# Optimization experiments

Hardware: AMD Instinct MI355X
Metric: run time of the kernel (lower is better)

## Reference

```python
import jax, jax.numpy as jnp
import numpy as np

L, H, D, FF = 6, 16, 768, 3072
B, N = 4, 1023
HD = D // H  # 48
EPS = 1e-5


def _layernorm(x, w, b):
    m = jnp.mean(x, axis=-1, keepdims=True)
    v = jnp.mean((x - m) ** 2, axis=-1, keepdims=True)
    return (x - m) / jnp.sqrt(v + EPS) * w + b


def setup_inputs() -> dict:
    key = jax.random.key(0)
    ks = jax.random.split(key, 10)
    ratio = 2.0 ** (-8.0 / H)
    slopes = np.array([ratio ** (i + 1) for i in range(H)], dtype=np.float32)
    return {
        "cls_tokens": jax.random.normal(ks[0], (B, N, D), jnp.float32),
        "cls_token": jax.random.normal(ks[1], (1, 1, D), jnp.float32) * 0.02,
        "log_slopes": jnp.log(jnp.asarray(slopes)),
        "Wqkv": jax.random.normal(ks[2], (L, 3 * D, D), jnp.float32) * 0.02,
        "Wo": jax.random.normal(ks[3], (L, D, D), jnp.float32) * 0.02,
        "Wg": jax.random.normal(ks[4], (L, FF, D), jnp.float32) * 0.02,
        "Wu": jax.random.normal(ks[5], (L, FF, D), jnp.float32) * 0.02,
        "Wd": jax.random.normal(ks[6], (L, D, FF), jnp.float32) * 0.02,
        "ln1_w": jnp.ones((L, D), jnp.float32),
        "ln1_b": jnp.zeros((L, D), jnp.float32),
        "ln2_w": jnp.ones((L, D), jnp.float32),
        "ln2_b": jnp.zeros((L, D), jnp.float32),
        "fin_w": jnp.ones((D,), jnp.float32),
        "fin_b": jnp.zeros((D,), jnp.float32),
    }


def reference(cls_tokens, cls_token, log_slopes, Wqkv, Wo, Wg, Wu, Wd,
              ln1_w, ln1_b, ln2_w, ln2_b, fin_w, fin_b):
    b, n, dmodel = cls_tokens.shape
    S = n + 1
    # learnable ALiBi: -exp(log_slope) * |i - j|, shape (H, S, S)
    pos = jnp.arange(S)
    dist = jnp.abs(pos[None, :] - pos[:, None]).astype(cls_tokens.dtype)
    bias = -(jnp.exp(log_slopes)[:, None, None] * dist[None, :, :])

    x = jnp.concatenate([jnp.broadcast_to(cls_token, (b, 1, dmodel)), cls_tokens], axis=1)
    scale = 1.0 / jnp.sqrt(jnp.asarray(HD, x.dtype))

    for l in range(L):
        h = _layernorm(x, ln1_w[l], ln1_b[l])
        qkv = jnp.einsum('bsd,ed->bse', h, Wqkv[l]).reshape(b, S, 3, H, HD)
        qkv = qkv.transpose(2, 0, 3, 1, 4)  # (3, B, H, S, hd)
        q, k, v = qkv[0], qkv[1], qkv[2]
        scores = jnp.einsum('bhqd,bhkd->bhqk', q, k) * scale + bias[None]
        attn = jax.nn.softmax(scores, axis=-1)
        o = jnp.einsum('bhqk,bhkd->bhqd', attn, v)
        o = o.transpose(0, 2, 1, 3).reshape(b, S, dmodel)
        x = x + jnp.einsum('bsd,ed->bse', o, Wo[l])
        h = _layernorm(x, ln2_w[l], ln2_b[l])
        gate = jax.nn.silu(jnp.einsum('bsd,fd->bsf', h, Wg[l]))
        up = jnp.einsum('bsd,fd->bsf', h, Wu[l])
        x = x + jnp.einsum('bsf,df->bsd', gate * up, Wd[l])

    return _layernorm(x[:, 0, :], fin_w, fin_b)
```

## Files before the change

kernel.cpp:

```cpp
#include <hip/hip_runtime.h>
#include <hip/hip_bf16.h>

#define LNUM 6
#define HNUM 16
#define DMODEL 768
#define FFDIM 3072
#define BATCH 4
#define NTOK 1023
#define SEQ 1024
#define HD 48
#define EPS 1e-5f

typedef __hip_bfloat16 bf16;

__device__ __forceinline__ unsigned short f2bf_raw(float f) {
  bf16 h = __float2bfloat16(f);
  union { bf16 h; unsigned short s; } u; u.h = h; return u.s;
}

template <int CTRL>
__device__ __forceinline__ float dppf(float x) {
  return __int_as_float(__builtin_amdgcn_update_dpp(
      0, __float_as_int(x), CTRL, 0xf, 0xf, true));
}
__device__ __forceinline__ float row_max16(float x) {
  x = fmaxf(x, dppf<0xB1>(x));
  x = fmaxf(x, dppf<0x4E>(x));
  x = fmaxf(x, dppf<0x124>(x));
  x = fmaxf(x, dppf<0x128>(x));
  return x;
}
__device__ __forceinline__ float row_sum16(float x) {
  x += dppf<0xB1>(x);
  x += dppf<0x4E>(x);
  x += dppf<0x124>(x);
  x += dppf<0x128>(x);
  return x;
}

__device__ __forceinline__ void xcd_swz(int& bx, int& by) {
  const int gx = gridDim.x;
  const int lin = blockIdx.y * gx + blockIdx.x;
  const int cpx = (gx * gridDim.y) >> 3;
  const int w = (lin & 7) * cpx + (lin >> 3);
  bx = w % gx;
  by = w / gx;
}

__global__ __launch_bounds__(256) void concat_kernel(
    const float* __restrict__ cls_tokens, const float* __restrict__ cls_token,
    float* __restrict__ x) {
  size_t i = (size_t)blockIdx.x * blockDim.x + threadIdx.x;
  const size_t total = (size_t)BATCH * SEQ * DMODEL;
  if (i >= total) return;
  int d = (int)(i % DMODEL);
  size_t bs = i / DMODEL;
  int s = (int)(bs % SEQ);
  int b = (int)(bs / SEQ);
  float v;
  if (s == 0) v = cls_token[d];
  else v = cls_tokens[((size_t)b * NTOK + (s - 1)) * DMODEL + d];
  x[i] = v;
}

#define W_QKV4  442368
#define W_O4    147456
#define W_FF4   589824
__global__ __launch_bounds__(256) void convert_w_kernel(
    const float* __restrict__ wqkv, const float* __restrict__ wo,
    const float* __restrict__ wg, const float* __restrict__ wu,
    const float* __restrict__ wd, bf16* __restrict__ dst) {
  size_t i4 = (size_t)blockIdx.x * 256 + threadIdx.x;
  size_t off4 = i4;
  const float* src;
  if (off4 < W_QKV4) src = wqkv;
  else { off4 -= W_QKV4;
    if (off4 < W_O4) src = wo;
    else { off4 -= W_O4;
      if (off4 < W_FF4) src = wg;
      else { off4 -= W_FF4;
        if (off4 < W_FF4) src = wu;
        else { off4 -= W_FF4; src = wd; } } } }
  float4 v = ((const float4*)src)[off4];
  ushort4 o;
  o.x = f2bf_raw(v.x); o.y = f2bf_raw(v.y);
  o.z = f2bf_raw(v.z); o.w = f2bf_raw(v.w);
  ((ushort4*)dst)[i4] = o;
}

__device__ __forceinline__ void st_ln(float* p, float v) { *p = v; }
__device__ __forceinline__ void st_ln(bf16* p, float v) { *p = __float2bfloat16(v); }

template <typename OUT>
__global__ __launch_bounds__(256) void ln_kernel(
    const float* __restrict__ in, OUT* __restrict__ out,
    const float* __restrict__ w, const float* __restrict__ bias,
    size_t in_stride, size_t out_stride) {
  const int row = blockIdx.x;
  const int tid = threadIdx.x;
  const float* x = in + (size_t)row * in_stride;
  OUT* y = out + (size_t)row * out_stride;

  float v0 = x[tid], v1 = x[tid + 256], v2 = x[tid + 512];
  float s = v0 + v1 + v2;
  float sq = v0 * v0 + v1 * v1 + v2 * v2;

  __shared__ float s_sum[256];
  __shared__ float s_sq[256];
  s_sum[tid] = s;
  s_sq[tid] = sq;
  __syncthreads();
  for (int off = 128; off > 0; off >>= 1) {
    if (tid < off) {
      s_sum[tid] += s_sum[tid + off];
      s_sq[tid] += s_sq[tid + off];
    }
    __syncthreads();
  }
  const float inv_d = 1.0f / (float)DMODEL;
  float mean = s_sum[0] * inv_d;
  float var = s_sq[0] * inv_d - mean * mean;
  float rstd = rsqrtf(var + EPS);

  st_ln(y + tid,       (v0 - mean) * rstd * w[tid]       + bias[tid]);
  st_ln(y + tid + 256, (v1 - mean) * rstd * w[tid + 256] + bias[tid + 256]);
  st_ln(y + tid + 512, (v2 - mean) * rstd * w[tid + 512] + bias[tid + 512]);
}

#define BM 128
#define BN 128
#define BK 32

typedef __attribute__((ext_vector_type(8))) short bfrag;
typedef __attribute__((ext_vector_type(4))) float f32x4;

__device__ __forceinline__ void async_copy16(const void* g, void* l) {
  __builtin_amdgcn_global_load_lds(
      (const __attribute__((address_space(1))) void*)g,
      (__attribute__((address_space(3))) void*)l, 16, 0, 0);
}

template <int CMODE>
__global__ __launch_bounds__(256) void gemm_bf16(
    const bf16* __restrict__ A, const bf16* __restrict__ B,
    void* __restrict__ Cv, int M, int N, int K) {
  __shared__ bf16 As[2][BM][BK];
  __shared__ bf16 Bs[2][BN][BK];

  const int tid = threadIdx.x;
  const int wave = tid >> 6;
  const int lane = tid & 63;
  int bx, by;
  xcd_swz(bx, by);
  const int m0 = by * BM;
  const int n0 = bx * BN;
  const int wm = (wave & 1) * 64;
  const int wn = (wave >> 1) * 64;

  f32x4 acc[4][4];
#pragma unroll
  for (int i = 0; i < 4; i++)
#pragma unroll
    for (int j = 0; j < 4; j++) acc[i][j] = (f32x4)(0.f);

  const int lrow = lane >> 2;
  const int lcol = (lane & 3) * 8;
  const bf16* Ag[2]; const bf16* Bg[2];
  void *AsB[2][2], *BsB[2][2];
#pragma unroll
  for (int j = 0; j < 2; j++) {
    int c = j * 4 + wave;
    Ag[j] = A + (size_t)(m0 + c * 16 + lrow) * K + lcol;
    Bg[j] = B + (size_t)(n0 + c * 16 + lrow) * K + lcol;
#pragma unroll
    for (int bf = 0; bf < 2; bf++) {
      AsB[bf][j] = (void*)&As[bf][c * 16][0];
      BsB[bf][j] = (void*)&Bs[bf][c * 16][0];
    }
  }

#pragma unroll
  for (int j = 0; j < 2; j++) {
    async_copy16(Ag[j], AsB[0][j]);
    async_copy16(Bg[j], BsB[0][j]);
  }

  const int fr = lane & 15;
  const int fk = (lane >> 4) * 8;
  const int nk = K / BK;

  for (int ki = 0; ki < nk; ki++) {
    const int cur = ki & 1;
    __syncthreads();
    if (ki + 1 < nk) {
      const int k0 = (ki + 1) * BK;
#pragma unroll
      for (int j = 0; j < 2; j++) {
        async_copy16(Ag[j] + k0, AsB[cur ^ 1][j]);
        async_copy16(Bg[j] + k0, BsB[cur ^ 1][j]);
      }
    }
    bfrag a[4], b[4];
#pragma unroll
    for (int i = 0; i < 4; i++) {
      a[i] = *(const bfrag*)&As[cur][wm + i * 16 + fr][fk];
      b[i] = *(const bfrag*)&Bs[cur][wn + i * 16 + fr][fk];
    }
#pragma unroll
    for (int i = 0; i < 4; i++)
#pragma unroll
      for (int j = 0; j < 4; j++)
        acc[i][j] = __builtin_amdgcn_mfma_f32_16x16x32_bf16(a[i], b[j], acc[i][j], 0, 0, 0);
  }

  const int ccol = lane & 15;
  const int crow = (lane >> 4) * 4;
#pragma unroll
  for (int i = 0; i < 4; i++) {
#pragma unroll
    for (int j = 0; j < 4; j++) {
#pragma unroll
      for (int r = 0; r < 4; r++) {
        const size_t gm = m0 + wm + i * 16 + crow + r;
        const size_t gn = n0 + wn + j * 16 + ccol;
        if (CMODE == 2) {
          ((bf16*)Cv)[gm * N + gn] = __float2bfloat16(acc[i][j][r]);
        } else if (CMODE == 1) {
          float* cp = (float*)Cv + gm * N + gn;
          *cp += acc[i][j][r];
        } else {
          ((float*)Cv)[gm * N + gn] = acc[i][j][r];
        }
      }
    }
  }
}

template <int CMODE, int SPLITK>
__global__ __launch_bounds__(256) void gemm_bf16_n64(
    const bf16* __restrict__ A, const bf16* __restrict__ B,
    void* __restrict__ Cv, int M, int N, int K) {
  __shared__ bf16 As[2][64][BK];
  __shared__ bf16 Bs[2][64][BK];

  const int tid = threadIdx.x;
  const int wave = tid >> 6;
  const int lane = tid & 63;
  int bx, by;
  xcd_swz(bx, by);
  const int m0 = by * 64;
  const int n0 = bx * 64;
  const int wm = (wave & 1) * 32;
  const int wn = (wave >> 1) * 32;
  const int koff = (SPLITK > 1) ? (int)blockIdx.z * (K / SPLITK) : 0;

  f32x4 acc[2][2];
#pragma unroll
  for (int i = 0; i < 2; i++)
#pragma unroll
    for (int j = 0; j < 2; j++) acc[i][j] = (f32x4)(0.f);

  const int srow = tid >> 2;
  const int scol = (tid & 3) * 8;
  const bf16* Ag = A + (size_t)(m0 + srow) * K + koff + scol;
  const bf16* Bg = B + (size_t)(n0 + srow) * K + koff + scol;
  void *AsB[2], *BsB[2];
#pragma unroll
  for (int bf = 0; bf < 2; bf++) {
    AsB[bf] = (void*)&As[bf][srow][scol];
    BsB[bf] = (void*)&Bs[bf][srow][scol];
  }

  async_copy16(Ag, AsB[0]);
  async_copy16(Bg, BsB[0]);

  const int fr = lane & 15;
  const int fk = (lane >> 4) * 8;
  const int nk = (K / SPLITK) / BK;

  for (int ki = 0; ki < nk; ki++) {
    const int cur = ki & 1;
    __syncthreads();
    if (ki + 1 < nk) {
      const int k0 = (ki + 1) * BK;
      async_copy16(Ag + k0, AsB[cur ^ 1]);
      async_copy16(Bg + k0, BsB[cur ^ 1]);
    }
    bfrag a[2], b[2];
#pragma unroll
    for (int i = 0; i < 2; i++)
      a[i] = *(const bfrag*)&As[cur][wm + i * 16 + fr][fk];
#pragma unroll
    for (int j = 0; j < 2; j++)
      b[j] = *(const bfrag*)&Bs[cur][wn + j * 16 + fr][fk];
#pragma unroll
    for (int i = 0; i < 2; i++)
#pragma unroll
      for (int j = 0; j < 2; j++)
        acc[i][j] = __builtin_amdgcn_mfma_f32_16x16x32_bf16(a[i], b[j], acc[i][j], 0, 0, 0);
  }

  const int ccol = lane & 15;
  const int crow = (lane >> 4) * 4;
#pragma unroll
  for (int i = 0; i < 2; i++) {
#pragma unroll
    for (int j = 0; j < 2; j++) {
#pragma unroll
      for (int r = 0; r < 4; r++) {
        const size_t gm = m0 + wm + i * 16 + crow + r;
        const size_t gn = n0 + wn + j * 16 + ccol;
        if (CMODE == 2) {
          ((bf16*)Cv)[gm * N + gn] = __float2bfloat16(acc[i][j][r]);
        } else if (CMODE == 1) {
          float* cp = (float*)Cv + gm * N + gn;
          if (SPLITK > 1) atomicAdd(cp, acc[i][j][r]);
          else *cp += acc[i][j][r];
        } else {
          ((float*)Cv)[gm * N + gn] = acc[i][j][r];
        }
      }
    }
  }
}

__global__ __launch_bounds__(256) void gemm_gateup(
    const bf16* __restrict__ A, const bf16* __restrict__ Wg,
    const bf16* __restrict__ Wu, bf16* __restrict__ gu, int M, int N, int K) {
  __shared__ bf16 As[2][BM][BK];
  __shared__ bf16 Gs[2][BN][BK];
  __shared__ bf16 Us[2][BN][BK];

  const int tid = threadIdx.x;
  const int wave = tid >> 6;
  const int lane = tid & 63;
  int bx, by;
  xcd_swz(bx, by);
  const int m0 = by * BM;
  const int n0 = bx * BN;
  const int wm = (wave & 1) * 64;
  const int wn = (wave >> 1) * 64;

  f32x4 accG[4][4], accU[4][4];
#pragma unroll
  for (int i = 0; i < 4; i++)
#pragma unroll
    for (int j = 0; j < 4; j++) { accG[i][j] = (f32x4)(0.f); accU[i][j] = (f32x4)(0.f); }

  const int lrow = lane >> 2;
  const int lcol = (lane & 3) * 8;
  const bf16 *Ag[2], *Gg[2], *Ug[2];
  void *AsB[2][2], *GsB[2][2], *UsB[2][2];
#pragma unroll
  for (int j = 0; j < 2; j++) {
    int c = j * 4 + wave;
    Ag[j] = A + (size_t)(m0 + c * 16 + lrow) * K + lcol;
    Gg[j] = Wg + (size_t)(n0 + c * 16 + lrow) * K + lcol;
    Ug[j] = Wu + (size_t)(n0 + c * 16 + lrow) * K + lcol;
#pragma unroll
    for (int bf = 0; bf < 2; bf++) {
      AsB[bf][j] = (void*)&As[bf][c * 16][0];
      GsB[bf][j] = (void*)&Gs[bf][c * 16][0];
      UsB[bf][j] = (void*)&Us[bf][c * 16][0];
    }
  }

#pragma unroll
  for (int j = 0; j < 2; j++) {
    async_copy16(Ag[j], AsB[0][j]);
    async_copy16(Gg[j], GsB[0][j]);
    async_copy16(Ug[j], UsB[0][j]);
  }

  const int fr = lane & 15;
  const int fk = (lane >> 4) * 8;
  const int nk = K / BK;

  for (int ki = 0; ki < nk; ki++) {
    const int cur = ki & 1;
    __syncthreads();
    if (ki + 1 < nk) {
      const int k0 = (ki + 1) * BK;
#pragma unroll
      for (int j = 0; j < 2; j++) {
        async_copy16(Ag[j] + k0, AsB[cur ^ 1][j]);
        async_copy16(Gg[j] + k0, GsB[cur ^ 1][j]);
        async_copy16(Ug[j] + k0, UsB[cur ^ 1][j]);
      }
    }
    bfrag a[4], g[4], u[4];
#pragma unroll
    for (int i = 0; i < 4; i++) {
      a[i] = *(const bfrag*)&As[cur][wm + i * 16 + fr][fk];
      g[i] = *(const bfrag*)&Gs[cur][wn + i * 16 + fr][fk];
      u[i] = *(const bfrag*)&Us[cur][wn + i * 16 + fr][fk];
    }
#pragma unroll
    for (int i = 0; i < 4; i++)
#pragma unroll
      for (int j = 0; j < 4; j++) {
        accG[i][j] = __builtin_amdgcn_mfma_f32_16x16x32_bf16(a[i], g[j], accG[i][j], 0, 0, 0);
        accU[i][j] = __builtin_amdgcn_mfma_f32_16x16x32_bf16(a[i], u[j], accU[i][j], 0, 0, 0);
      }
  }

  const int ccol = lane & 15;
  const int crow = (lane >> 4) * 4;
#pragma unroll
  for (int i = 0; i < 4; i++) {
#pragma unroll
    for (int j = 0; j < 4; j++) {
#pragma unroll
      for (int r = 0; r < 4; r++) {
        const size_t gm = m0 + wm + i * 16 + crow + r;
        const size_t gn = n0 + wn + j * 16 + ccol;
        const float gv = accG[i][j][r];
        const float uv = accU[i][j][r];
        const float res = gv / (1.0f + __expf(-gv)) * uv;
        gu[gm * N + gn] = __float2bfloat16(res);
      }
    }
  }
}

__global__ __launch_bounds__(256) void transpose_v(
    const bf16* __restrict__ qkv, bf16* __restrict__ vt) {
  __shared__ bf16 T[HD][64];
  const int tid = threadIdx.x;
  const int kb = blockIdx.x * 64;
  const int h = blockIdx.y;
  const int b = blockIdx.z;
  const size_t rstride = 3 * DMODEL;
  const bf16* vsrc = qkv + ((size_t)(b * SEQ + kb)) * rstride + 2 * DMODEL + h * HD;

  if (tid < 192) {
    int p = tid & 31, c = tid >> 5;
    const bf16* v0 = vsrc + (size_t)(2 * p) * rstride + c * 8;
    uint4 r0 = *(const uint4*)v0;
    uint4 r1 = *(const uint4*)(v0 + rstride);
    const unsigned int* w0 = (const unsigned int*)&r0;
    const unsigned int* w1 = (const unsigned int*)&r1;
#pragma unroll
    for (int i = 0; i < 8; i++) {
      unsigned int lo = (i & 1) ? (w0[i >> 1] >> 16) : (w0[i >> 1] & 0xffffu);
      unsigned int hi = (i & 1) ? (w1[i >> 1] >> 16) : (w1[i >> 1] & 0xffffu);
      *(unsigned int*)&T[c * 8 + i][2 * p] = lo | (hi << 16);
    }
  }
  __syncthreads();
  for (int it = tid; it < HD * 8; it += 256) {
    int d = it >> 3, c = it & 7;
    *(uint4*)(vt + ((size_t)((b * HNUM + h) * HD + d)) * SEQ + kb + c * 8) =
        *(const uint4*)&T[d][c * 8];
  }
}

#define AQT 64
#define AKT 64
#define ASTR 72

__global__ __launch_bounds__(256, 4) void attn_mfma(
    const bf16* __restrict__ qkv, const bf16* __restrict__ vt,
    const float* __restrict__ log_slopes, bf16* __restrict__ obuf) {
  __shared__ bf16 QPs[AQT][ASTR];
  __shared__ bf16 Ks[AKT][ASTR];
  __shared__ bf16 Vs[HD][ASTR];

  const int tid = threadIdx.x;
  const int wq = tid >> 6;
  const int lane = tid & 63;
  const int l15 = lane & 15;
  const int lh = lane >> 4;

  const int id = blockIdx.x;
  const int w = (id & 7) * 128 + (id >> 3);
  const int qb = (w & 15) * AQT;
  const int h = (w >> 4) & 15;
  const int b = w >> 8;

  const float c1 = 0.14433756729740643f * 1.4426950408889634f;
  const float slope2 = __expf(log_slopes[h]) * 1.4426950408889634f;
  const size_t rstride = 3 * DMODEL;
  const bf16* qbase = qkv + ((size_t)(b * SEQ + qb)) * rstride + h * HD;
  const bf16* kbase0 = qkv + ((size_t)b * SEQ) * rstride + DMODEL + h * HD;
  const bf16* vbase0 = vt + ((size_t)((b * HNUM + h) * HD)) * SEQ;

  bf16* ldst[3];
  int goff[3];
  bool isK[3];
#pragma unroll
  for (int j = 0; j < 3; j++) {
    int id2 = tid + j * 256;
    if (id2 < 384) {
      int r = id2 / 6, c = id2 - r * 6;
      ldst[j] = &Ks[r][c * 8];
      goff[j] = r * (int)rstride + c * 8;
      isK[j] = true;
    } else {
      id2 -= 384;
      int d = id2 >> 3, c = id2 & 7;
      ldst[j] = &Vs[d][c * 8];
      goff[j] = d * SEQ + c * 8;
      isK[j] = false;
    }
  }

  for (int it = tid; it < AQT * 2; it += 256) {
    int r = it >> 1, c = it & 1;
    *(uint4*)&QPs[r][48 + c * 8] = make_uint4(0, 0, 0, 0);
    *(uint4*)&Ks[r][48 + c * 8] = make_uint4(0, 0, 0, 0);
  }
  for (int it = tid; it < AQT * 6; it += 256) {
    int r = it / 6, c = it - (it / 6) * 6;
    *(uint4*)&QPs[r][c * 8] = *(const uint4*)(qbase + (size_t)r * rstride + c * 8);
  }
  __syncthreads();
  const bfrag aq0 = *(const bfrag*)&QPs[wq * 16 + l15][lh * 8];
  const bfrag aq1 = *(const bfrag*)&QPs[wq * 16 + l15][32 + lh * 8];

  uint4 pre[3];
#pragma unroll
  for (int j = 0; j < 3; j++)
    pre[j] = *(const uint4*)((isK[j] ? kbase0 : vbase0) + goff[j]);

  float m_[4], l_[4];
  f32x4 accO[3];
#pragma unroll
  for (int r = 0; r < 4; r++) { m_[r] = -1e30f; l_[r] = 0.f; }
#pragma unroll
  for (int t = 0; t < 3; t++) accO[t] = (f32x4)(0.f);

  for (int kb = 0; kb < SEQ; kb += AKT) {
    __syncthreads();
#pragma unroll
    for (int j = 0; j < 3; j++) *(uint4*)ldst[j] = pre[j];
    __syncthreads();
    if (kb + AKT < SEQ) {
      const bf16* kb1 = kbase0 + (size_t)(kb + AKT) * rstride;
      const bf16* vb1 = vbase0 + (kb + AKT);
#pragma unroll
      for (int j = 0; j < 3; j++)
        pre[j] = *(const uint4*)((isK[j] ? kb1 : vb1) + goff[j]);
    }

    f32x4 accS[4];
#pragma unroll
    for (int j = 0; j < 4; j++) accS[j] = (f32x4)(0.f);
    __builtin_amdgcn_s_setprio(1);
#pragma unroll
    for (int j = 0; j < 4; j++) {
      bfrag bk = *(const bfrag*)&Ks[j * 16 + l15][lh * 8];
      accS[j] = __builtin_amdgcn_mfma_f32_16x16x32_bf16(aq0, bk, accS[j], 0, 0, 0);
    }
#pragma unroll
    for (int j = 0; j < 4; j++) {
      bfrag bk = *(const bfrag*)&Ks[j * 16 + l15][32 + lh * 8];
      accS[j] = __builtin_amdgcn_mfma_f32_16x16x32_bf16(aq1, bk, accS[j], 0, 0, 0);
    }
    __builtin_amdgcn_s_setprio(0);

    float ps[4][4];
#pragma unroll
    for (int r = 0; r < 4; r++) {
      const float fq = (float)(qb + wq * 16 + lh * 4 + r);
      float s[4];
#pragma unroll
      for (int j = 0; j < 4; j++) {
        const float fk = (float)(kb + j * 16 + l15);
        s[j] = fmaf(accS[j][r], c1, -slope2 * fabsf(fq - fk));
      }
      float mx = row_max16(fmaxf(fmaxf(s[0], s[1]), fmaxf(s[2], s[3])));
      if (!__all(mx - m_[r] <= 8.0f)) {
        const float mnew = fmaxf(m_[r], mx);
        const float corr = exp2f(m_[r] - mnew);
        l_[r] *= corr;
#pragma unroll
        for (int t = 0; t < 3; t++) accO[t][r] *= corr;
        m_[r] = mnew;
      }
      float rs = 0.f;
#pragma unroll
      for (int j = 0; j < 4; j++) {
        ps[j][r] = exp2f(s[j] - m_[r]);
        rs += ps[j][r];
      }
      rs = row_sum16(rs);
      l_[r] += rs;
    }

#pragma unroll
    for (int j = 0; j < 4; j++)
#pragma unroll
      for (int r = 0; r < 4; r++)
        QPs[wq * 16 + lh * 4 + r][j * 16 + l15] = __float2bfloat16(ps[j][r]);

#pragma unroll
    for (int ks = 0; ks < 2; ks++) {
      bfrag pa = *(const bfrag*)&QPs[wq * 16 + l15][ks * 32 + lh * 8];
      __builtin_amdgcn_s_setprio(1);
#pragma unroll
      for (int t = 0; t < 3; t++) {
        bfrag vb = *(const bfrag*)&Vs[t * 16 + l15][ks * 32 + lh * 8];
        accO[t] = __builtin_amdgcn_mfma_f32_16x16x32_bf16(pa, vb, accO[t], 0, 0, 0);
      }
      __builtin_amdgcn_s_setprio(0);
    }
  }

#pragma unroll
  for (int r = 0; r < 4; r++) {
    const float inv = 1.0f / l_[r];
    bf16* op = obuf + ((size_t)(b * SEQ + qb + wq * 16 + lh * 4 + r)) * DMODEL + h * HD;
#pragma unroll
    for (int t = 0; t < 3; t++)
      op[t * 16 + l15] = __float2bfloat16(accO[t][r] * inv);
  }
}

extern "C" void kernel_launch(void* const* d_in, const int* in_sizes, int n_in,
                              void* d_out, int out_size, void* d_ws, size_t ws_size,
                              hipStream_t stream) {
  const float* cls_tokens = (const float*)d_in[0];
  const float* cls_token  = (const float*)d_in[1];
  const float* log_slopes = (const float*)d_in[2];
  const float* Wqkv = (const float*)d_in[3];
  const float* Wo   = (const float*)d_in[4];
  const float* Wg   = (const float*)d_in[5];
  const float* Wu   = (const float*)d_in[6];
  const float* Wd   = (const float*)d_in[7];
  const float* ln1_w = (const float*)d_in[8];
  const float* ln1_b = (const float*)d_in[9];
  const float* ln2_w = (const float*)d_in[10];
  const float* ln2_b = (const float*)d_in[11];
  const float* fin_w = (const float*)d_in[12];
  const float* fin_b = (const float*)d_in[13];
  float* out = (float*)d_out;

  const size_t ROWS = (size_t)BATCH * SEQ;
  char* wsb = (char*)d_ws;
  float* x    = (float*)(wsb);
  bf16* qkvb  = (bf16*)(wsb + 12582912);
  bf16* hb    = (bf16*)(wsb + 31457280);
  bf16* ob    = (bf16*)(wsb + 37748736);
  bf16* gub   = (bf16*)(wsb + 44040192);
  bf16* wbf   = (bf16*)(wsb + 94371840);
  bf16* vtb   = (bf16*)(wsb + 113246208);

  bf16* wqkv_b = wbf;
  bf16* wo_b   = wbf + 1769472;
  bf16* wg_b   = wbf + 2359296;
  bf16* wu_b   = wbf + 4718592;
  bf16* wd_b   = wbf + 7077888;

  {
    const size_t total = ROWS * DMODEL;
    concat_kernel<<<(int)((total + 255) / 256), 256, 0, stream>>>(cls_tokens, cls_token, x);
  }

  for (int l = 0; l < LNUM; l++) {
    convert_w_kernel<<<9216, 256, 0, stream>>>(
        Wqkv + (size_t)l * 3 * DMODEL * DMODEL, Wo + (size_t)l * DMODEL * DMODEL,
        Wg + (size_t)l * FFDIM * DMODEL, Wu + (size_t)l * FFDIM * DMODEL,
        Wd + (size_t)l * DMODEL * FFDIM, wbf);

    ln_kernel<bf16><<<(int)ROWS, 256, 0, stream>>>(
        x, hb, ln1_w + l * DMODEL, ln1_b + l * DMODEL, DMODEL, DMODEL);
    gemm_bf16<2><<<dim3(3 * DMODEL / BN, ROWS / BM), 256, 0, stream>>>(
        hb, wqkv_b, qkvb, (int)ROWS, 3 * DMODEL, DMODEL);
    transpose_v<<<dim3(SEQ / 64, HNUM, BATCH), 256, 0, stream>>>(qkvb, vtb);
    attn_mfma<<<dim3(SEQ / AQT * HNUM * BATCH), 256, 0, stream>>>(
        qkvb, vtb, log_slopes, ob);
    gemm_bf16_n64<1, 1><<<dim3(DMODEL / 64, ROWS / 64), 256, 0, stream>>>(
        ob, wo_b, x, (int)ROWS, DMODEL, DMODEL);
    ln_kernel<bf16><<<(int)ROWS, 256, 0, stream>>>(
        x, hb, ln2_w + l * DMODEL, ln2_b + l * DMODEL, DMODEL, DMODEL);
    gemm_gateup<<<dim3(FFDIM / BN, ROWS / BM), 256, 0, stream>>>(
        hb, wg_b, wu_b, gub, (int)ROWS, FFDIM, DMODEL);
    gemm_bf16_n64<1, 2><<<dim3(DMODEL / 64, ROWS / 64, 2), 256, 0, stream>>>(
        gub, wd_b, x, (int)ROWS, DMODEL, FFDIM);
  }

  ln_kernel<float><<<BATCH, 256, 0, stream>>>(x, out, fin_w, fin_b,
                                              (size_t)SEQ * DMODEL, DMODEL);
}
```

Before: 1.765 ms.

## Split attention over KV halves, widen n64 GEMM tile, warp-per-row layernorm

Attention blocks now each process half of the key/value sequence and write unnormalized fp32 partial outputs plus running max/sum. A new combine kernel merges the two halves and writes bf16. This doubles the number of attention blocks for better occupancy, at the cost of extra fp32 traffic and one more launch. The n64 GEMM now uses 128-row tiles, and the Wo projection switches to split-K with atomic adds. Layernorm assigns one wave per row with float4 loads and shuffle reductions, replacing the shared-memory tree reduction.

```diff
diff --git a/kernel.cpp b/kernel.cpp
--- a/kernel.cpp
+++ b/kernel.cpp
@@ -88,43 +88,55 @@
   ((ushort4*)dst)[i4] = o;
 }
 
-__device__ __forceinline__ void st_ln(float* p, float v) { *p = v; }
-__device__ __forceinline__ void st_ln(bf16* p, float v) { *p = __float2bfloat16(v); }
+__device__ __forceinline__ void st4(float* p, float a, float b2, float c, float d) {
+  *(float4*)p = make_float4(a, b2, c, d);
+}
+__device__ __forceinline__ void st4(bf16* p, float a, float b2, float c, float d) {
+  ushort4 o;
+  o.x = f2bf_raw(a); o.y = f2bf_raw(b2); o.z = f2bf_raw(c); o.w = f2bf_raw(d);
+  *(ushort4*)p = o;
+}
 
 template <typename OUT>
 __global__ __launch_bounds__(256) void ln_kernel(
     const float* __restrict__ in, OUT* __restrict__ out,
     const float* __restrict__ w, const float* __restrict__ bias,
-    size_t in_stride, size_t out_stride) {
-  const int row = blockIdx.x;
-  const int tid = threadIdx.x;
+    size_t in_stride, size_t out_stride, int nrows) {
+  const int lane = threadIdx.x & 63;
+  const int row = blockIdx.x * 4 + (threadIdx.x >> 6);
+  if (row >= nrows) return;
   const float* x = in + (size_t)row * in_stride;
   OUT* y = out + (size_t)row * out_stride;
-
-  float v0 = x[tid], v1 = x[tid + 256], v2 = x[tid + 512];
-  float s = v0 + v1 + v2;
-  float sq = v0 * v0 + v1 * v1 + v2 * v2;
-
-  __shared__ float s_sum[256];
-  __shared__ float s_sq[256];
-  s_sum[tid] = s;
-  s_sq[tid] = sq;
-  __syncthreads();
-  for (int off = 128; off > 0; off >>= 1) {
-    if (tid < off) {
-      s_sum[tid] += s_sum[tid + off];
-      s_sq[tid] += s_sq[tid + off];
-    }
-    __syncthreads();
-  }
+  const int d = lane * 4;
+
+  float4 v0 = *(const float4*)(x + d);
+  float4 v1 = *(const float4*)(x + d + 256);
+  float4 v2 = *(const float4*)(x + d + 512);
+  float s = (v0.x + v0.y) + (v0.z + v0.w) + (v1.x + v1.y) + (v1.z + v1.w) +
+            (v2.x + v2.y) + (v2.z + v2.w);
+  float sq = v0.x * v0.x + v0.y * v0.y + v0.z * v0.z + v0.w * v0.w +
+             v1.x * v1.x + v1.y * v1.y + v1.z * v1.z + v1.w * v1.w +
+             v2.x * v2.x + v2.y * v2.y + v2.z * v2.z + v2.w * v2.w;
+  s = row_sum16(s);  s += __shfl_xor(s, 16, 64);  s += __shfl_xor(s, 32, 64);
+  sq = row_sum16(sq); sq += __shfl_xor(sq, 16, 64); sq += __shfl_xor(sq, 32, 64);
+
   const float inv_d = 1.0f / (float)DMODEL;
-  float mean = s_sum[0] * inv_d;
-  float var = s_sq[0] * inv_d - mean * mean;
-  float rstd = rsqrtf(var + EPS);
-
-  st_ln(y + tid,       (v0 - mean) * rstd * w[tid]       + bias[tid]);
-  st_ln(y + tid + 256, (v1 - mean) * rstd * w[tid + 256] + bias[tid + 256]);
-  st_ln(y + tid + 512, (v2 - mean) * rstd * w[tid + 512] + bias[tid + 512]);
+  const float mean = s * inv_d;
+  const float var = sq * inv_d - mean * mean;
+  const float rstd = rsqrtf(var + EPS);
+
+  float4 w0 = *(const float4*)(w + d);
+  float4 b0 = *(const float4*)(bias + d);
+  st4(y + d, (v0.x - mean) * rstd * w0.x + b0.x, (v0.y - mean) * rstd * w0.y + b0.y,
+             (v0.z - mean) * rstd * w0.z + b0.z, (v0.w - mean) * rstd * w0.w + b0.w);
+  float4 w1 = *(const float4*)(w + d + 256);
+  float4 b1 = *(const float4*)(bias + d + 256);
+  st4(y + d + 256, (v1.x - mean) * rstd * w1.x + b1.x, (v1.y - mean) * rstd * w1.y + b1.y,
+                   (v1.z - mean) * rstd * w1.z + b1.z, (v1.w - mean) * rstd * w1.w + b1.w);
+  float4 w2 = *(const float4*)(w + d + 512);
+  float4 b2 = *(const float4*)(bias + d + 512);
+  st4(y + d + 512, (v2.x - mean) * rstd * w2.x + b2.x, (v2.y - mean) * rstd * w2.y + b2.y,
+                   (v2.z - mean) * rstd * w2.z + b2.z, (v2.w - mean) * rstd * w2.w + b2.w);
 }
 
 #define BM 128
@@ -236,11 +248,11 @@
   }
 }
 
-template <int CMODE, int SPLITK>
+template <int SPLITK>
 __global__ __launch_bounds__(256) void gemm_bf16_n64(
     const bf16* __restrict__ A, const bf16* __restrict__ B,
-    void* __restrict__ Cv, int M, int N, int K) {
-  __shared__ bf16 As[2][64][BK];
+    float* __restrict__ Cv, int M, int N, int K) {
+  __shared__ bf16 As[2][BM][BK];
   __shared__ bf16 Bs[2][64][BK];
 
   const int tid = threadIdx.x;
@@ -248,30 +260,35 @@
   const int lane = tid & 63;
   int bx, by;
   xcd_swz(bx, by);
-  const int m0 = by * 64;
+  const int m0 = by * BM;
   const int n0 = bx * 64;
-  const int wm = (wave & 1) * 32;
+  const int wm = (wave & 1) * 64;
   const int wn = (wave >> 1) * 32;
   const int koff = (SPLITK > 1) ? (int)blockIdx.z * (K / SPLITK) : 0;
 
-  f32x4 acc[2][2];
-#pragma unroll
-  for (int i = 0; i < 2; i++)
+  f32x4 acc[4][2];
+#pragma unroll
+  for (int i = 0; i < 4; i++)
 #pragma unroll
     for (int j = 0; j < 2; j++) acc[i][j] = (f32x4)(0.f);
 
-  const int srow = tid >> 2;
-  const int scol = (tid & 3) * 8;
-  const bf16* Ag = A + (size_t)(m0 + srow) * K + koff + scol;
-  const bf16* Bg = B + (size_t)(n0 + srow) * K + koff + scol;
-  void *AsB[2], *BsB[2];
-#pragma unroll
-  for (int bf = 0; bf < 2; bf++) {
-    AsB[bf] = (void*)&As[bf][srow][scol];
-    BsB[bf] = (void*)&Bs[bf][srow][scol];
-  }
-
-  async_copy16(Ag, AsB[0]);
+  const int lrow = lane >> 2;
+  const int lcol = (lane & 3) * 8;
+  const bf16* Ag[2]; const bf16* Bg;
+  void *AsB[2][2], *BsB[2];
+#pragma unroll
+  for (int j = 0; j < 2; j++) {
+    int c = j * 4 + wave;
+    Ag[j] = A + (size_t)(m0 + c * 16 + lrow) * K + koff + lcol;
+#pragma unroll
+    for (int bf = 0; bf < 2; bf++) AsB[bf][j] = (void*)&As[bf][c * 16][0];
+  }
+  Bg = B + (size_t)(n0 + wave * 16 + lrow) * K + koff + lcol;
+#pragma unroll
+  for (int bf = 0; bf < 2; bf++) BsB[bf] = (void*)&Bs[bf][wave * 16][0];
+
+  async_copy16(Ag[0], AsB[0][0]);
+  async_copy16(Ag[1], AsB[0][1]);
   async_copy16(Bg, BsB[0]);
 
   const int fr = lane & 15;
@@ -283,18 +300,19 @@
     __syncthreads();
     if (ki + 1 < nk) {
       const int k0 = (ki + 1) * BK;
-      async_copy16(Ag + k0, AsB[cur ^ 1]);
+      async_copy16(Ag[0] + k0, AsB[cur ^ 1][0]);
+      async_copy16(Ag[1] + k0, AsB[cur ^ 1][1]);
       async_copy16(Bg + k0, BsB[cur ^ 1]);
     }
-    bfrag a[2], b[2];
-#pragma unroll
-    for (int i = 0; i < 2; i++)
+    bfrag a[4], b[2];
+#pragma unroll
+    for (int i = 0; i < 4; i++)
       a[i] = *(const bfrag*)&As[cur][wm + i * 16 + fr][fk];
 #pragma unroll
     for (int j = 0; j < 2; j++)
       b[j] = *(const bfrag*)&Bs[cur][wn + j * 16 + fr][fk];
 #pragma unroll
-    for (int i = 0; i < 2; i++)
+    for (int i = 0; i < 4; i++)
 #pragma unroll
       for (int j = 0; j < 2; j++)
         acc[i][j] = __builtin_amdgcn_mfma_f32_16x16x32_bf16(a[i], b[j], acc[i][j], 0, 0, 0);
@@ -303,22 +321,16 @@
   const int ccol = lane & 15;
   const int crow = (lane >> 4) * 4;
 #pragma unroll
-  for (int i = 0; i < 2; i++) {
+  for (int i = 0; i < 4; i++) {
 #pragma unroll
     for (int j = 0; j < 2; j++) {
 #pragma unroll
       for (int r = 0; r < 4; r++) {
         const size_t gm = m0 + wm + i * 16 + crow + r;
         const size_t gn = n0 + wn + j * 16 + ccol;
-        if (CMODE == 2) {
-          ((bf16*)Cv)[gm * N + gn] = __float2bfloat16(acc[i][j][r]);
-        } else if (CMODE == 1) {
-          float* cp = (float*)Cv + gm * N + gn;
-          if (SPLITK > 1) atomicAdd(cp, acc[i][j][r]);
-          else *cp += acc[i][j][r];
-        } else {
-          ((float*)Cv)[gm * N + gn] = acc[i][j][r];
-        }
+        float* cp = Cv + gm * N + gn;
+        if (SPLITK > 1) atomicAdd(cp, acc[i][j][r]);
+        else *cp += acc[i][j][r];
       }
     }
   }
@@ -458,10 +470,12 @@
 #define AQT 64
 #define AKT 64
 #define ASTR 72
+#define KVH 512
 
 __global__ __launch_bounds__(256, 4) void attn_mfma(
     const bf16* __restrict__ qkv, const bf16* __restrict__ vt,
-    const float* __restrict__ log_slopes, bf16* __restrict__ obuf) {
+    const float* __restrict__ log_slopes,
+    float* __restrict__ po, float2* __restrict__ ml) {
   __shared__ bf16 QPs[AQT][ASTR];
   __shared__ bf16 Ks[AKT][ASTR];
   __shared__ bf16 Vs[HD][ASTR];
@@ -473,17 +487,21 @@
   const int lh = lane >> 4;
 
   const int id = blockIdx.x;
-  const int w = (id & 7) * 128 + (id >> 3);
-  const int qb = (w & 15) * AQT;
-  const int h = (w >> 4) & 15;
-  const int b = w >> 8;
+  const int w = (id & 7) * 256 + (id >> 3);
+  const int kvhalf = w & 1;
+  const int unit = w >> 1;
+  const int qb = (unit & 15) * AQT;
+  const int h = (unit >> 4) & 15;
+  const int b = unit >> 8;
+  const int kv0 = kvhalf * KVH;
+  const int kvend = kv0 + KVH;
 
   const float c1 = 0.14433756729740643f * 1.4426950408889634f;
   const float slope2 = __expf(log_slopes[h]) * 1.4426950408889634f;
   const size_t rstride = 3 * DMODEL;
   const bf16* qbase = qkv + ((size_t)(b * SEQ + qb)) * rstride + h * HD;
-  const bf16* kbase0 = qkv + ((size_t)b * SEQ) * rstride + DMODEL + h * HD;
-  const bf16* vbase0 = vt + ((size_t)((b * HNUM + h) * HD)) * SEQ;
+  const bf16* kbase0 = qkv + ((size_t)(b * SEQ + kv0)) * rstride + DMODEL + h * HD;
+  const bf16* vbase0 = vt + ((size_t)((b * HNUM + h) * HD)) * SEQ + kv0;
 
   bf16* ldst[3];
   int goff[3];
@@ -530,14 +548,14 @@
 #pragma unroll
   for (int t = 0; t < 3; t++) accO[t] = (f32x4)(0.f);
 
-  for (int kb = 0; kb < SEQ; kb += AKT) {
+  for (int kb = kv0; kb < kvend; kb += AKT) {
     __syncthreads();
 #pragma unroll
     for (int j = 0; j < 3; j++) *(uint4*)ldst[j] = pre[j];
     __syncthreads();
-    if (kb + AKT < SEQ) {
-      const bf16* kb1 = kbase0 + (size_t)(kb + AKT) * rstride;
-      const bf16* vb1 = vbase0 + (kb + AKT);
+    if (kb + AKT < kvend) {
+      const bf16* kb1 = kbase0 + (size_t)(kb + AKT - kv0) * rstride;
+      const bf16* vb1 = vbase0 + (kb + AKT - kv0);
 #pragma unroll
       for (int j = 0; j < 3; j++)
         pre[j] = *(const uint4*)((isK[j] ? kb1 : vb1) + goff[j]);
@@ -607,14 +625,53 @@
     }
   }
 
+  const size_t hbase = (size_t)kvhalf * BATCH * SEQ;
 #pragma unroll
   for (int r = 0; r < 4; r++) {
-    const float inv = 1.0f / l_[r];
-    bf16* op = obuf + ((size_t)(b * SEQ + qb + wq * 16 + lh * 4 + r)) * DMODEL + h * HD;
+    const int row = qb + wq * 16 + lh * 4 + r;
+    float* op = po + (hbase + b * SEQ + row) * DMODEL + h * HD;
 #pragma unroll
     for (int t = 0; t < 3; t++)
-      op[t * 16 + l15] = __float2bfloat16(accO[t][r] * inv);
-  }
+      op[t * 16 + l15] = accO[t][r];
+    if (l15 == 0)
+      ml[(hbase + b * SEQ + row) * HNUM + h] = make_float2(m_[r], l_[r]);
+  }
+}
+
+__global__ __launch_bounds__(256) void attn_combine(
+    const float* __restrict__ po, const float2* __restrict__ ml,
+    bf16* __restrict__ obuf) {
+  const int tid = threadIdx.x;
+  const int rh = blockIdx.x * 64 + (tid >> 2);
+  const int q4 = tid & 3;
+  const int bs = rh >> 4;
+  const int h = rh & 15;
+
+  const float2 ml0 = ml[rh];
+  const float2 ml1 = ml[BATCH * SEQ * HNUM + rh];
+  const float m = fmaxf(ml0.x, ml1.x);
+  const float w0 = exp2f(ml0.x - m);
+  const float w1 = exp2f(ml1.x - m);
+  const float inv = 1.0f / (ml0.y * w0 + ml1.y * w1);
+
+  const size_t base = (size_t)bs * DMODEL + h * HD + q4 * 12;
+  const float* p0 = po + base;
+  const float* p1 = po + (size_t)BATCH * SEQ * DMODEL + base;
+  unsigned int ow[6];
+#pragma unroll
+  for (int i = 0; i < 3; i++) {
+    float4 a = *(const float4*)(p0 + i * 4);
+    float4 c = *(const float4*)(p1 + i * 4);
+    const float o0 = (a.x * w0 + c.x * w1) * inv;
+    const float o1 = (a.y * w0 + c.y * w1) * inv;
+    const float o2 = (a.z * w0 + c.z * w1) * inv;
+    const float o3 = (a.w * w0 + c.w * w1) * inv;
+    ow[i * 2]     = (unsigned)f2bf_raw(o0) | ((unsigned)f2bf_raw(o1) << 16);
+    ow[i * 2 + 1] = (unsigned)f2bf_raw(o2) | ((unsigned)f2bf_raw(o3) << 16);
+  }
+  unsigned int* op = (unsigned int*)(obuf + base);
+#pragma unroll
+  for (int i = 0; i < 6; i++) op[i] = ow[i];
 }
 
 extern "C" void kernel_launch(void* const* d_in, const int* in_sizes, int n_in,
@@ -646,6 +703,9 @@
   bf16* wbf   = (bf16*)(wsb + 94371840);
   bf16* vtb   = (bf16*)(wsb + 113246208);
 
+  float* po = (float*)gub;
+  float2* mlb = (float2*)hb;
+
   bf16* wqkv_b = wbf;
   bf16* wo_b   = wbf + 1769472;
   bf16* wg_b   = wbf + 2359296;
@@ -663,23 +723,24 @@
         Wg + (size_t)l * FFDIM * DMODEL, Wu + (size_t)l * FFDIM * DMODEL,
         Wd + (size_t)l * DMODEL * FFDIM, wbf);
 
-    ln_kernel<bf16><<<(int)ROWS, 256, 0, stream>>>(
-        x, hb, ln1_w + l * DMODEL, ln1_b + l * DMODEL, DMODEL, DMODEL);
+    ln_kernel<bf16><<<(int)(ROWS / 4), 256, 0, stream>>>(
+        x, hb, ln1_w + l * DMODEL, ln1_b + l * DMODEL, DMODEL, DMODEL, (int)ROWS);
     gemm_bf16<2><<<dim3(3 * DMODEL / BN, ROWS / BM), 256, 0, stream>>>(
         hb, wqkv_b, qkvb, (int)ROWS, 3 * DMODEL, DMODEL);
     transpose_v<<<dim3(SEQ / 64, HNUM, BATCH), 256, 0, stream>>>(qkvb, vtb);
-    attn_mfma<<<dim3(SEQ / AQT * HNUM * BATCH), 256, 0, stream>>>(
-        qkvb, vtb, log_slopes, ob);
-    gemm_bf16_n64<1, 1><<<dim3(DMODEL / 64, ROWS / 64), 256, 0, stream>>>(
+    attn_mfma<<<dim3(2 * SEQ / AQT * HNUM * BATCH), 256, 0, stream>>>(
+        qkvb, vtb, log_slopes, po, mlb);
+    attn_combine<<<(int)(ROWS * HNUM / 64), 256, 0, stream>>>(po, mlb, ob);
+    gemm_bf16_n64<2><<<dim3(DMODEL / 64, ROWS / BM, 2), 256, 0, stream>>>(
         ob, wo_b, x, (int)ROWS, DMODEL, DMODEL);
-    ln_kernel<bf16><<<(int)ROWS, 256, 0, stream>>>(
-        x, hb, ln2_w + l * DMODEL, ln2_b + l * DMODEL, DMODEL, DMODEL);
+    ln_kernel<bf16><<<(int)(ROWS / 4), 256, 0, stream>>>(
+        x, hb, ln2_w + l * DMODEL, ln2_b + l * DMODEL, DMODEL, DMODEL, (int)ROWS);
     gemm_gateup<<<dim3(FFDIM / BN, ROWS / BM), 256, 0, stream>>>(
         hb, wg_b, wu_b, gub, (int)ROWS, FFDIM, DMODEL);
-    gemm_bf16_n64<1, 2><<<dim3(DMODEL / 64, ROWS / 64, 2), 256, 0, stream>>>(
+    gemm_bf16_n64<2><<<dim3(DMODEL / 64, ROWS / BM, 2), 256, 0, stream>>>(
         gub, wd_b, x, (int)ROWS, DMODEL, FFDIM);
   }
 
-  ln_kernel<float><<<BATCH, 256, 0, stream>>>(x, out, fin_w, fin_b,
-                                              (size_t)SEQ * DMODEL, DMODEL);
-}
+  ln_kernel<float><<<1, 256, 0, stream>>>(x, out, fin_w, fin_b,
+                                          (size_t)SEQ * DMODEL, DMODEL, BATCH);
+}
```

Result: slower. 1.818 ms (+3.0%).
